# Kernel tuning notes

Hardware: AMD Instinct MI355X
Metric: run time of the kernel (lower is better)

Reference implementation:

```python
import jax, jax.numpy as jnp
import numpy as np

EPS_NORM = 1e-12  # F.normalize eps
EPS_BN = 1e-5     # BatchNorm1d eps


def _gather_neighbors(tensor, index):
    # tensor: (bs, v, d), index: (bs, v, n) -> (bs, v, n, d)
    return jax.vmap(lambda t, i: t[i])(tensor, index)


def setup_inputs() -> dict:
    key = jax.random.key(0)
    ks = jax.random.split(key, 8)
    bs, v, n = 4, 4096, 32
    cin, cout = 128, 256
    stdv = float(np.sqrt(2.0 / cout))
    return {
        "neighbor_index": jax.random.randint(ks[0], (bs, v, n), 0, v),
        "vertices": jax.random.normal(ks[1], (bs, v, 3), dtype=jnp.float32),
        "feature_map": jax.random.normal(ks[2], (bs, v, cin - 1), dtype=jnp.float32),
        "directions": jax.random.uniform(ks[3], (4, cout), minval=-stdv, maxval=stdv, dtype=jnp.float32),
        "W": jax.random.normal(ks[4], (cout, cin), dtype=jnp.float32) / np.sqrt(cin),
        "b": jnp.zeros((cout,), jnp.float32),
        "gamma": jnp.ones((cout,), jnp.float32),
        "beta": jnp.zeros((cout,), jnp.float32),
    }


def reference(neighbor_index, vertices, feature_map, directions, W, b, gamma, beta):
    # --- direction-based weights theta: (bs, v, n, cout) ---
    neighbors = _gather_neighbors(vertices, neighbor_index)          # (bs,v,n,3)
    direc = neighbors - vertices[:, :, None, :]
    direc_norm = direc / jnp.maximum(
        jnp.linalg.norm(direc, axis=-1, keepdims=True), EPS_NORM)    # F.normalize
    dir_w = (direc_norm + 1.0) * 0.5                                  # (bs,v,n,3)
    sup_w = jnp.stack([directions[1] - directions[0],
                       directions[2] - directions[0],
                       directions[3] - directions[0]], axis=0)        # (3, cout)
    theta = jax.nn.relu(jnp.einsum('bvnk,kc->bvnc', dir_w, sup_w) + directions[0])

    # --- gathered features + L2 distance channel ---
    fs = _gather_neighbors(feature_map, neighbor_index)               # (bs,v,n,cin-1)
    fdist = jnp.sqrt(jnp.sum(fs * fs, axis=-1, keepdims=True))        # (bs,v,n,1)
    fs = jnp.concatenate([fs, fdist], axis=-1)                        # (bs,v,n,cin)

    # --- Linear -> BatchNorm1d (training stats) -> ReLU ---
    z = jnp.einsum('bvni,ci->bvnc', fs, W) + b                        # (bs,v,n,cout)
    mean = jnp.mean(z, axis=(0, 1, 2))
    var = jnp.mean(jnp.square(z - mean), axis=(0, 1, 2))              # biased var
    zn = (z - mean) * jax.lax.rsqrt(var + EPS_BN) * gamma + beta
    act = jax.nn.relu(zn) * theta

    # --- max-pool over neighbor dim ---
    return jnp.max(act, axis=2)                                       # (bs,v,cout)
```

## Files before the change

### kernel.cpp

```cpp
#include <hip/hip_runtime.h>

typedef unsigned short ushort_t;
typedef __attribute__((ext_vector_type(8))) short short8;
typedef __attribute__((ext_vector_type(4))) float floatx4;
typedef __attribute__((ext_vector_type(2))) float floatx2;

#define NN    32
#define CIN   128
#define COUT  256
#define NPTS  16384
#define NSAMP (NPTS * NN)
#define LDA   136
#define HB    128

__device__ __align__(16) ushort_t g_wb[COUT * CIN];
__device__ __align__(16) ushort_t g_y[(size_t)NPTS * COUT];
__device__ __align__(16) int      g_hp[HB * 4096];
__device__ __align__(16) float    g_sp[256 * 512];
__device__ __align__(16) float    g_consts[1536];

__device__ __forceinline__ float bf2f(ushort_t u) {
    return __uint_as_float(((unsigned int)u) << 16);
}
__device__ __forceinline__ ushort_t f2bf(float f) {
    unsigned int x = __float_as_uint(f);
    return (ushort_t)((x + 0x7FFFu + ((x >> 16) & 1u)) >> 16);
}
__device__ __forceinline__ int probe_f32(const void* verts, int lane) {
    float ax = fabsf(bf2f(((const ushort_t*)verts)[lane]));
    unsigned long long b = __ballot((ax > 1e-5f) && (ax < 32.0f));
    return (__popcll(b) >= 56) ? 0 : 1;
}
__device__ __forceinline__ float lanebcast(float v, int jj) {
    return __uint_as_float((unsigned)__builtin_amdgcn_readlane(__float_as_int(v), jj));
}

__global__ __launch_bounds__(256)
void hist_kernel(const int* __restrict__ nbr,
                 const void* __restrict__ Wg,
                 const void* __restrict__ verts) {
    __shared__ int h[4096];
    const int b   = blockIdx.x;
    const int tid = threadIdx.x;
    if (b < HB) {
        #pragma unroll
        for (int i = 0; i < 16; ++i) h[i * 256 + tid] = 0;
        __syncthreads();
        const int* src = nbr + (size_t)b * 4096;
        #pragma unroll
        for (int i = 0; i < 16; ++i) atomicAdd(&h[src[i * 256 + tid]], 1);
        __syncthreads();
        int* dst = g_hp + (size_t)b * 4096;
        #pragma unroll
        for (int i = 0; i < 16; ++i) dst[i * 256 + tid] = h[i * 256 + tid];
    } else {
        const int f32 = probe_f32(verts, tid & 63);
        int i = (b - HB) * 1024 + tid * 4;
        if (f32) {
            float4 v = ((const float4*)Wg)[i >> 2];
            g_wb[i] = f2bf(v.x); g_wb[i + 1] = f2bf(v.y);
            g_wb[i + 2] = f2bf(v.z); g_wb[i + 3] = f2bf(v.w);
        } else {
            *(uint2*)(g_wb + i) = *(const uint2*)((const ushort_t*)Wg + i);
        }
    }
}

__global__ __launch_bounds__(256, 2)
void ygemm_kernel(const void* __restrict__ fm, const void* __restrict__ verts) {
    __shared__ __align__(16) ushort_t At[64 * LDA];
    __shared__ float multS[64];

    const int tid  = threadIdx.x;
    const int r0   = blockIdx.x * 64;
    const int lane = tid & 63;
    const int f32  = probe_f32(verts, lane);

    if (tid < 64) {
        const int* hp = g_hp + (size_t)(r0 >> 12) * 32 * 4096 + (r0 & 4095) + tid;
        int s = 0;
        #pragma unroll
        for (int p2 = 0; p2 < 32; ++p2) s += hp[(size_t)p2 * 4096];
        multS[tid] = (float)s;
    }

    const int rl4 = tid >> 6;
    #pragma unroll 4
    for (int i = 0; i < 16; ++i) {
        const int rl = i * 4 + rl4;
        float f0, f1; ushort_t u0, u1;
        if (f32) {
            const float* src = (const float*)fm + (size_t)(r0 + rl) * 127;
            f0 = src[lane];
            f1 = (lane < 63) ? src[64 + lane] : 0.0f;
            u0 = f2bf(f0); u1 = f2bf(f1);
        } else {
            const ushort_t* src = (const ushort_t*)fm + (size_t)(r0 + rl) * 127;
            u0 = src[lane];
            u1 = (lane < 63) ? src[64 + lane] : (ushort_t)0;
            f0 = bf2f(u0); f1 = bf2f(u1);
        }
        float ss = f0 * f0 + f1 * f1;
        #pragma unroll
        for (int d = 1; d < 64; d <<= 1) ss += __shfl_xor(ss, d, 64);
        At[rl * LDA + lane]      = u0;
        At[rl * LDA + 64 + lane] = (lane < 63) ? u1 : f2bf(sqrtf(ss));
    }
    __syncthreads();

    const int w = tid >> 6;
    const int m = lane & 15;
    const int q = lane >> 4;

    floatx4 acc[4][4];
    #pragma unroll
    for (int rt = 0; rt < 4; ++rt)
        #pragma unroll
        for (int ct = 0; ct < 4; ++ct)
            acc[rt][ct] = (floatx4){0.0f, 0.0f, 0.0f, 0.0f};

    #pragma unroll
    for (int kk = 0; kk < 4; ++kk) {
        const int kof = kk * 32 + q * 8;
        short8 af[4];
        #pragma unroll
        for (int rt = 0; rt < 4; ++rt)
            af[rt] = *(const short8*)&At[(rt * 16 + m) * LDA + kof];
        short8 bfr[4];
        #pragma unroll
        for (int ct = 0; ct < 4; ++ct) {
            int ch = w * 64 + ct * 16 + m;
            bfr[ct] = *(const short8*)(g_wb + ch * CIN + kof);
        }
        #pragma unroll
        for (int rt = 0; rt < 4; ++rt)
            #pragma unroll
            for (int ct = 0; ct < 4; ++ct)
                acc[rt][ct] = __builtin_amdgcn_mfma_f32_16x16x32_bf16(
                    af[rt], bfr[ct], acc[rt][ct], 0, 0, 0);
    }

    #pragma unroll
    for (int ct = 0; ct < 4; ++ct) {
        const int ch = w * 64 + ct * 16 + m;
        float s = 0.0f, ss = 0.0f;
        #pragma unroll
        for (int rt = 0; rt < 4; ++rt)
            #pragma unroll
            for (int j = 0; j < 4; ++j) {
                int rloc = rt * 16 + q * 4 + j;
                ushort_t yb = f2bf(acc[rt][ct][j]);
                g_y[(size_t)(r0 + rloc) * COUT + ch] = yb;
                float yv = bf2f(yb);
                float wm = multS[rloc];
                s  += wm * yv;
                ss += wm * yv * yv;
            }
        s  += __shfl_xor(s, 16, 64);  s  += __shfl_xor(s, 32, 64);
        ss += __shfl_xor(ss, 16, 64); ss += __shfl_xor(ss, 32, 64);
        if (q == 0) {
            g_sp[(size_t)blockIdx.x * 512 + ch]       = s;
            g_sp[(size_t)blockIdx.x * 512 + 256 + ch] = ss;
        }
    }
}

__global__ void finalize_kernel(const void* __restrict__ gamma,
                                const void* __restrict__ beta,
                                const void* __restrict__ dirs,
                                const void* __restrict__ verts) {
    const int c   = threadIdx.x;
    const int f32 = probe_f32(verts, c & 63);

    float s = 0.0f, ss = 0.0f;
    #pragma unroll 8
    for (int p2 = 0; p2 < 256; ++p2) {
        s  += g_sp[(size_t)p2 * 512 + c];
        ss += g_sp[(size_t)p2 * 512 + 256 + c];
    }
    const float invN = 1.0f / (float)NSAMP;
    float mean = s * invN;
    float var  = fmaxf(ss * invN - mean * mean, 0.0f);
    float inv  = 1.0f / sqrtf(var + 1e-5f);
    float ga, be, d0, d1, d2, d3;
    if (f32) {
        ga = ((const float*)gamma)[c]; be = ((const float*)beta)[c];
        const float* dd = (const float*)dirs;
        d0 = dd[c]; d1 = dd[256 + c]; d2 = dd[512 + c]; d3 = dd[768 + c];
    } else {
        ga = bf2f(((const ushort_t*)gamma)[c]); be = bf2f(((const ushort_t*)beta)[c]);
        const ushort_t* dd = (const ushort_t*)dirs;
        d0 = bf2f(dd[c]); d1 = bf2f(dd[256 + c]);
        d2 = bf2f(dd[512 + c]); d3 = bf2f(dd[768 + c]);
    }
    float scale = ga * inv;
    g_consts[c]        = scale;
    g_consts[256 + c]  = be - mean * scale;
    g_consts[512 + c]  = d0;
    g_consts[768 + c]  = d1 - d0;
    g_consts[1024 + c] = d2 - d0;
    g_consts[1280 + c] = d3 - d0;
}

__global__ __launch_bounds__(256, 5)
void epi_kernel(const int* __restrict__ nbr,
                const void* __restrict__ verts,
                void* __restrict__ out) {
    const int tid  = threadIdx.x;
    const int lane = tid & 63;
    const int bid  = blockIdx.x;
    const int p0   = (((bid & 7) << 9) | (bid >> 3)) << 2;
    const int p    = p0 + (tid >> 6);
    const int f32  = probe_f32(verts, lane);
    const int j    = lane & 31;

    int   gv;
    float wx, wy, wz;
    {
        gv = ((p >> 12) << 12) + nbr[(size_t)p * NN + j];
        float sx, sy, sz, nx, ny, nz;
        if (f32) {
            const float* vv = (const float*)verts;
            sx = vv[p * 3]; sy = vv[p * 3 + 1]; sz = vv[p * 3 + 2];
            nx = vv[gv * 3]; ny = vv[gv * 3 + 1]; nz = vv[gv * 3 + 2];
        } else {
            const ushort_t* vv = (const ushort_t*)verts;
            sx = bf2f(vv[p * 3]); sy = bf2f(vv[p * 3 + 1]); sz = bf2f(vv[p * 3 + 2]);
            nx = bf2f(vv[gv * 3]); ny = bf2f(vv[gv * 3 + 1]); nz = bf2f(vv[gv * 3 + 2]);
        }
        float dx = nx - sx, dy = ny - sy, dz = nz - sz;
        float nrm = sqrtf(dx * dx + dy * dy + dz * dz);
        float inv = 1.0f / fmaxf(nrm, 1e-12f);
        wx = (dx * inv + 1.0f) * 0.5f;
        wy = (dy * inv + 1.0f) * 0.5f;
        wz = (dz * inv + 1.0f) * 0.5f;
    }

    const int c4 = lane * 4;
    const floatx4 zero = {0.0f, 0.0f, 0.0f, 0.0f};
    const floatx4 sc = *(const floatx4*)&g_consts[c4];
    const floatx4 sh = *(const floatx4*)&g_consts[256 + c4];
    const floatx4 d0 = *(const floatx4*)&g_consts[512 + c4];
    const floatx4 s0 = *(const floatx4*)&g_consts[768 + c4];
    const floatx4 s1 = *(const floatx4*)&g_consts[1024 + c4];
    const floatx4 s2 = *(const floatx4*)&g_consts[1280 + c4];

    floatx4 vmA = zero, vmB = zero;
    uint2 u[8];

    #pragma unroll
    for (int k = 0; k < 8; ++k) {
        int r = __builtin_amdgcn_readlane(gv, k);
        u[k] = *(const uint2*)(g_y + ((size_t)(unsigned)r << 8) + c4);
    }
    #pragma unroll
    for (int g = 0; g < 4; ++g) {
        #pragma unroll
        for (int k = 0; k < 8; ++k) {
            const int jj = g * 8 + k;
            const uint2 uk = u[k];
            if (g < 3) {
                int r = __builtin_amdgcn_readlane(gv, jj + 8);
                u[k] = *(const uint2*)(g_y + ((size_t)(unsigned)r << 8) + c4);
            }
            float wxs = lanebcast(wx, jj);
            float wys = lanebcast(wy, jj);
            float wzs = lanebcast(wz, jj);
            floatx4 y;
            y.x = __uint_as_float(uk.x << 16);
            y.y = __uint_as_float(uk.x & 0xFFFF0000u);
            y.z = __uint_as_float(uk.y << 16);
            y.w = __uint_as_float(uk.y & 0xFFFF0000u);
            floatx4 th = d0 + s0 * wxs + s1 * wys + s2 * wzs;
            th = __builtin_elementwise_max(th, zero);
            floatx4 zt = (y * sc + sh) * th;
            if (k & 1) vmB = __builtin_elementwise_max(vmB, zt);
            else       vmA = __builtin_elementwise_max(vmA, zt);
        }
    }
    floatx4 vm = __builtin_elementwise_max(vmA, vmB);

    size_t ofs = (size_t)p * COUT + c4;
    if (f32) {
        *(floatx4*)((float*)out + ofs) = vm;
    } else {
        uint2 ou;
        ou.x = ((unsigned int)f2bf(vm.y) << 16) | (unsigned int)f2bf(vm.x);
        ou.y = ((unsigned int)f2bf(vm.w) << 16) | (unsigned int)f2bf(vm.z);
        *(uint2*)((ushort_t*)out + ofs) = ou;
    }
}

extern "C" void kernel_launch(void* const* d_in, const int* in_sizes, int n_in,
                              void* d_out, int out_size, void* d_ws, size_t ws_size,
                              hipStream_t stream) {
    const int* nbr    = (const int*)d_in[0];
    const void* verts = d_in[1];
    const void* fm    = d_in[2];
    const void* dirs  = d_in[3];
    const void* Wg    = d_in[4];
    const void* gamma = d_in[6];
    const void* beta  = d_in[7];
    (void)d_ws; (void)ws_size; (void)in_sizes; (void)n_in; (void)out_size;

    hist_kernel<<<dim3(HB + 32), dim3(256), 0, stream>>>(nbr, Wg, verts);
    ygemm_kernel<<<dim3(NPTS / 64), dim3(256), 0, stream>>>(fm, verts);
    finalize_kernel<<<dim3(1), dim3(256), 0, stream>>>(gamma, beta, dirs, verts);
    epi_kernel<<<dim3(NPTS / 4), dim3(256), 0, stream>>>(nbr, verts, d_out);
}
```

Measured before the change: 140.5 us.

## Split wavefront halves across neighbors with 16-byte row loads in epilogue

Result: no change. 140.9 us (+0.3%).

```diff
diff --git a/kernel.cpp b/kernel.cpp
--- a/kernel.cpp
+++ b/kernel.cpp
@@ -31,8 +31,8 @@
     unsigned long long b = __ballot((ax > 1e-5f) && (ax < 32.0f));
     return (__popcll(b) >= 56) ? 0 : 1;
 }
-__device__ __forceinline__ float lanebcast(float v, int jj) {
-    return __uint_as_float((unsigned)__builtin_amdgcn_readlane(__float_as_int(v), jj));
+__device__ __forceinline__ float bperm_f(int abytes, float v) {
+    return __uint_as_float((unsigned)__builtin_amdgcn_ds_bpermute(abytes, __float_as_int(v)));
 }
 
 __global__ __launch_bounds__(256)
@@ -202,7 +202,7 @@
     g_consts[1280 + c] = d3 - d0;
 }
 
-__global__ __launch_bounds__(256, 5)
+__global__ __launch_bounds__(256, 4)
 void epi_kernel(const int* __restrict__ nbr,
                 const void* __restrict__ verts,
                 void* __restrict__ out) {
@@ -236,58 +236,100 @@
         wz = (dz * inv + 1.0f) * 0.5f;
     }
 
-    const int c4 = lane * 4;
+    const int hsel = (lane >> 5) << 2;
+    const int cofs = (lane & 31) << 4;
+    const int c8   = (lane & 31) * 8;
+
     const floatx4 zero = {0.0f, 0.0f, 0.0f, 0.0f};
-    const floatx4 sc = *(const floatx4*)&g_consts[c4];
-    const floatx4 sh = *(const floatx4*)&g_consts[256 + c4];
-    const floatx4 d0 = *(const floatx4*)&g_consts[512 + c4];
-    const floatx4 s0 = *(const floatx4*)&g_consts[768 + c4];
-    const floatx4 s1 = *(const floatx4*)&g_consts[1024 + c4];
-    const floatx4 s2 = *(const floatx4*)&g_consts[1280 + c4];
-
-    floatx4 vmA = zero, vmB = zero;
-    uint2 u[8];
-
-    #pragma unroll
-    for (int k = 0; k < 8; ++k) {
-        int r = __builtin_amdgcn_readlane(gv, k);
-        u[k] = *(const uint2*)(g_y + ((size_t)(unsigned)r << 8) + c4);
+    const floatx4 scL = *(const floatx4*)&g_consts[c8];
+    const floatx4 scH = *(const floatx4*)&g_consts[c8 + 4];
+    const floatx4 shL = *(const floatx4*)&g_consts[256 + c8];
+    const floatx4 shH = *(const floatx4*)&g_consts[256 + c8 + 4];
+    const floatx4 d0L = *(const floatx4*)&g_consts[512 + c8];
+    const floatx4 d0H = *(const floatx4*)&g_consts[512 + c8 + 4];
+    const floatx4 s0L = *(const floatx4*)&g_consts[768 + c8];
+    const floatx4 s0H = *(const floatx4*)&g_consts[768 + c8 + 4];
+    const floatx4 s1L = *(const floatx4*)&g_consts[1024 + c8];
+    const floatx4 s1H = *(const floatx4*)&g_consts[1024 + c8 + 4];
+    const floatx4 s2L = *(const floatx4*)&g_consts[1280 + c8];
+    const floatx4 s2H = *(const floatx4*)&g_consts[1280 + c8 + 4];
+
+    const char* gyb = (const char*)g_y;
+    floatx4 aL0 = zero, aH0 = zero, aL1 = zero, aH1 = zero;
+    uint4 u[4]; float bx[4], by[4], bz[4];
+
+    #pragma unroll
+    for (int k = 0; k < 4; ++k) {
+        const int av = k * 8 + hsel;
+        int rw = __builtin_amdgcn_ds_bpermute(av, gv);
+        bx[k] = bperm_f(av, wx);
+        by[k] = bperm_f(av, wy);
+        bz[k] = bperm_f(av, wz);
+        u[k] = *(const uint4*)(gyb + (((unsigned)rw << 9) + (unsigned)cofs));
     }
     #pragma unroll
     for (int g = 0; g < 4; ++g) {
         #pragma unroll
-        for (int k = 0; k < 8; ++k) {
-            const int jj = g * 8 + k;
-            const uint2 uk = u[k];
+        for (int k = 0; k < 4; ++k) {
+            const uint4 uk = u[k];
+            const float wxs = bx[k], wys = by[k], wzs = bz[k];
             if (g < 3) {
-                int r = __builtin_amdgcn_readlane(gv, jj + 8);
-                u[k] = *(const uint2*)(g_y + ((size_t)(unsigned)r << 8) + c4);
+                const int av = (g * 4 + k + 4) * 8 + hsel;
+                int rw = __builtin_amdgcn_ds_bpermute(av, gv);
+                bx[k] = bperm_f(av, wx);
+                by[k] = bperm_f(av, wy);
+                bz[k] = bperm_f(av, wz);
+                u[k] = *(const uint4*)(gyb + (((unsigned)rw << 9) + (unsigned)cofs));
             }
-            float wxs = lanebcast(wx, jj);
-            float wys = lanebcast(wy, jj);
-            float wzs = lanebcast(wz, jj);
-            floatx4 y;
-            y.x = __uint_as_float(uk.x << 16);
-            y.y = __uint_as_float(uk.x & 0xFFFF0000u);
-            y.z = __uint_as_float(uk.y << 16);
-            y.w = __uint_as_float(uk.y & 0xFFFF0000u);
-            floatx4 th = d0 + s0 * wxs + s1 * wys + s2 * wzs;
-            th = __builtin_elementwise_max(th, zero);
-            floatx4 zt = (y * sc + sh) * th;
-            if (k & 1) vmB = __builtin_elementwise_max(vmB, zt);
-            else       vmA = __builtin_elementwise_max(vmA, zt);
-        }
-    }
-    floatx4 vm = __builtin_elementwise_max(vmA, vmB);
-
-    size_t ofs = (size_t)p * COUT + c4;
-    if (f32) {
-        *(floatx4*)((float*)out + ofs) = vm;
-    } else {
-        uint2 ou;
-        ou.x = ((unsigned int)f2bf(vm.y) << 16) | (unsigned int)f2bf(vm.x);
-        ou.y = ((unsigned int)f2bf(vm.w) << 16) | (unsigned int)f2bf(vm.z);
-        *(uint2*)((ushort_t*)out + ofs) = ou;
+            floatx4 yL, yH;
+            yL.x = __uint_as_float(uk.x << 16);
+            yL.y = __uint_as_float(uk.x & 0xFFFF0000u);
+            yL.z = __uint_as_float(uk.y << 16);
+            yL.w = __uint_as_float(uk.y & 0xFFFF0000u);
+            yH.x = __uint_as_float(uk.z << 16);
+            yH.y = __uint_as_float(uk.z & 0xFFFF0000u);
+            yH.z = __uint_as_float(uk.w << 16);
+            yH.w = __uint_as_float(uk.w & 0xFFFF0000u);
+            floatx4 thL = d0L + s0L * wxs + s1L * wys + s2L * wzs;
+            floatx4 thH = d0H + s0H * wxs + s1H * wys + s2H * wzs;
+            thL = __builtin_elementwise_max(thL, zero);
+            thH = __builtin_elementwise_max(thH, zero);
+            floatx4 ztL = (yL * scL + shL) * thL;
+            floatx4 ztH = (yH * scH + shH) * thH;
+            if (k & 1) {
+                aL1 = __builtin_elementwise_max(aL1, ztL);
+                aH1 = __builtin_elementwise_max(aH1, ztH);
+            } else {
+                aL0 = __builtin_elementwise_max(aL0, ztL);
+                aH0 = __builtin_elementwise_max(aH0, ztH);
+            }
+        }
+    }
+    floatx4 vL = __builtin_elementwise_max(aL0, aL1);
+    floatx4 vH = __builtin_elementwise_max(aH0, aH1);
+
+    vL.x = fmaxf(vL.x, __shfl_xor(vL.x, 32, 64));
+    vL.y = fmaxf(vL.y, __shfl_xor(vL.y, 32, 64));
+    vL.z = fmaxf(vL.z, __shfl_xor(vL.z, 32, 64));
+    vL.w = fmaxf(vL.w, __shfl_xor(vL.w, 32, 64));
+    vH.x = fmaxf(vH.x, __shfl_xor(vH.x, 32, 64));
+    vH.y = fmaxf(vH.y, __shfl_xor(vH.y, 32, 64));
+    vH.z = fmaxf(vH.z, __shfl_xor(vH.z, 32, 64));
+    vH.w = fmaxf(vH.w, __shfl_xor(vH.w, 32, 64));
+
+    if (lane < 32) {
+        size_t ofs = (size_t)p * COUT + c8;
+        if (f32) {
+            *(floatx4*)((float*)out + ofs)     = vL;
+            *(floatx4*)((float*)out + ofs + 4) = vH;
+        } else {
+            uint4 ou;
+            ou.x = ((unsigned int)f2bf(vL.y) << 16) | (unsigned int)f2bf(vL.x);
+            ou.y = ((unsigned int)f2bf(vL.w) << 16) | (unsigned int)f2bf(vL.z);
+            ou.z = ((unsigned int)f2bf(vH.y) << 16) | (unsigned int)f2bf(vH.x);
+            ou.w = ((unsigned int)f2bf(vH.w) << 16) | (unsigned int)f2bf(vH.z);
+            *(uint4*)((ushort_t*)out + ofs) = ou;
+        }
     }
 }
 
```
